# Kernel tuning notes

Hardware: AMD Instinct MI355X
Metric: run time of the kernel (lower is better)

Reference implementation:

```python
import jax, jax.numpy as jnp
import numpy as np

IN_FEATURES = 3
OUT_FEATURES = 256
WEIGHT_SCALE = 1.0
ALPHA = 6.0


def setup_inputs() -> dict:
    key = jax.random.key(0)
    k_x, k_w, k_b, k_mu, k_g = jax.random.split(key, 5)
    B, N = 4, 65536
    # coordinates in [-1, 1], matching mu's init range
    x = jax.random.uniform(k_x, (B, N, IN_FEATURES), jnp.float32, -1.0, 1.0)
    # gamma ~ Gamma(alpha, 1)
    gamma = jax.random.gamma(k_g, ALPHA, (OUT_FEATURES,), jnp.float32)
    # linear weight init (Kaiming-uniform-like) then scaled by weight_scale * sqrt(gamma)
    bound = 1.0 / np.sqrt(IN_FEATURES)
    W = jax.random.uniform(k_w, (OUT_FEATURES, IN_FEATURES), jnp.float32, -bound, bound)
    W = W * (WEIGHT_SCALE * jnp.sqrt(gamma)[:, None])
    # bias ~ U(-pi, pi)
    b = jax.random.uniform(k_b, (OUT_FEATURES,), jnp.float32, -np.pi, np.pi)
    # mu ~ U(-1, 1), stored as (out, in) (the (1,1,out,in) singleton dims are pure broadcast)
    mu = jax.random.uniform(k_mu, (OUT_FEATURES, IN_FEATURES), jnp.float32, -1.0, 1.0)
    return {"x": x, "W": W, "b": b, "mu": mu, "gamma": gamma}


def reference(x, W, b, mu, gamma):
    # linear: (B, N, out)
    lin = jnp.einsum("bnd,od->bno", x, W) + b
    x2 = jnp.sum(x * x, axis=-1, keepdims=True)          # (B, N, 1)
    mu2 = jnp.sum(mu * mu, axis=-1)                       # (out,)
    cross = jnp.einsum("bnd,od->bno", x, mu)             # (B, N, out)
    D = x2 - 2.0 * cross + mu2                            # (B, N, out)
    return jnp.sin(lin) * jnp.exp(-0.5 * D * gamma)
```

## Files before the change

### kernel.cpp

```cpp
#include <hip/hip_runtime.h>


#define OUT_FEATURES 256

__global__ __launch_bounds__(256) void gabor_kernel(
    const float* __restrict__ x,
    const float* __restrict__ W,
    const float* __restrict__ b,
    const float* __restrict__ mu,
    const float* __restrict__ gamma,
    float* __restrict__ out,
    int P)
{
    const int lane        = threadIdx.x & 63;
    const int waveInBlock = threadIdx.x >> 6;
    const int wavesPerBlk = blockDim.x >> 6;
    const int waveId      = blockIdx.x * wavesPerBlk + waveInBlock;
    const int wavesTotal  = gridDim.x * wavesPerBlk;

    const int o = lane << 2;

    float w0[4], w1[4], w2[4], bb[4], m0[4], m1[4], m2[4], mu2s[4], gs[4];
#pragma unroll
    for (int j = 0; j < 4; ++j) {
        const int oj = o + j;
        w0[j] = W[oj * 3 + 0];
        w1[j] = W[oj * 3 + 1];
        w2[j] = W[oj * 3 + 2];
        m0[j] = mu[oj * 3 + 0];
        m1[j] = mu[oj * 3 + 1];
        m2[j] = mu[oj * 3 + 2];
        bb[j] = b[oj];
        gs[j] = -0.5f * gamma[oj];
        mu2s[j] = m0[j] * m0[j] + m1[j] * m1[j] + m2[j] * m2[j];
    }

    for (int p = waveId; p < P; p += wavesTotal) {
        const float x0 = x[p * 3 + 0];
        const float x1 = x[p * 3 + 1];
        const float x2 = x[p * 3 + 2];
        const float xs = x0 * x0 + x1 * x1 + x2 * x2;

        float4 r;
        float* rp = &r.x;
#pragma unroll
        for (int j = 0; j < 4; ++j) {
            const float lin   = fmaf(w0[j], x0, fmaf(w1[j], x1, fmaf(w2[j], x2, bb[j])));
            const float cross = fmaf(m0[j], x0, fmaf(m1[j], x1, m2[j] * x2));
            const float D     = xs - 2.0f * cross + mu2s[j];
            rp[j] = __sinf(lin) * __expf(gs[j] * D);
        }

        *reinterpret_cast<float4*>(out + (size_t)p * OUT_FEATURES + o) = r;
    }
}

extern "C" void kernel_launch(void* const* d_in, const int* in_sizes, int n_in,
                              void* d_out, int out_size, void* d_ws, size_t ws_size,
                              hipStream_t stream) {
    const float* x     = (const float*)d_in[0];
    const float* W     = (const float*)d_in[1];
    const float* b     = (const float*)d_in[2];
    const float* mu    = (const float*)d_in[3];
    const float* gamma = (const float*)d_in[4];
    float* out = (float*)d_out;

    const int P = in_sizes[0] / 3;

    const int blocks = 2048;
    gabor_kernel<<<blocks, 256, 0, stream>>>(x, W, b, mu, gamma, out, P);
}
```

Measured before the change: 283.0 us.

## Use nontemporal output stores, scalar x loads, vector param loads, more blocks

Output stores become nontemporal vector stores so the large write-only result bypasses cache retention. The per-point index is made wave-uniform with readfirstlane so the x loads can become scalar loads. Parameters are now read with 16-byte vector loads. The grid doubles to 4096 blocks and launch bounds request 4 blocks per CU. The kernel is write-bandwidth bound (256 MB of output), so the gain depends mainly on the nontemporal store behaviour.

```diff
diff --git a/kernel.cpp b/kernel.cpp
--- a/kernel.cpp
+++ b/kernel.cpp
@@ -1,9 +1,11 @@
 #include <hip/hip_runtime.h>
 
 
-#define OUT_FEATURES 256
+#define OUT_F 256
 
-__global__ __launch_bounds__(256) void gabor_kernel(
+typedef float v4f __attribute__((ext_vector_type(4)));
+
+__global__ __launch_bounds__(256, 4) void gabor_kernel(
     const float* __restrict__ x,
     const float* __restrict__ W,
     const float* __restrict__ b,
@@ -15,43 +17,49 @@
     const int lane        = threadIdx.x & 63;
     const int waveInBlock = threadIdx.x >> 6;
     const int wavesPerBlk = blockDim.x >> 6;
+    const int wavesTotal  = gridDim.x * wavesPerBlk;
     const int waveId      = blockIdx.x * wavesPerBlk + waveInBlock;
-    const int wavesTotal  = gridDim.x * wavesPerBlk;
 
     const int o = lane << 2;
 
-    float w0[4], w1[4], w2[4], bb[4], m0[4], m1[4], m2[4], mu2s[4], gs[4];
+    float wv[12], mv[12];
+    {
+        const v4f* Wp = (const v4f*)(W + o * 3);
+        const v4f* Mp = (const v4f*)(mu + o * 3);
+#pragma unroll
+        for (int i = 0; i < 3; ++i) {
+            v4f wq = Wp[i], mq = Mp[i];
+#pragma unroll
+            for (int j = 0; j < 4; ++j) { wv[i * 4 + j] = wq[j]; mv[i * 4 + j] = mq[j]; }
+        }
+    }
+    const v4f bq = *(const v4f*)(b + o);
+    const v4f gq = *(const v4f*)(gamma + o);
+
+    float bb[4], gs[4], mu2s[4];
 #pragma unroll
     for (int j = 0; j < 4; ++j) {
-        const int oj = o + j;
-        w0[j] = W[oj * 3 + 0];
-        w1[j] = W[oj * 3 + 1];
-        w2[j] = W[oj * 3 + 2];
-        m0[j] = mu[oj * 3 + 0];
-        m1[j] = mu[oj * 3 + 1];
-        m2[j] = mu[oj * 3 + 2];
-        bb[j] = b[oj];
-        gs[j] = -0.5f * gamma[oj];
-        mu2s[j] = m0[j] * m0[j] + m1[j] * m1[j] + m2[j] * m2[j];
+        bb[j] = bq[j];
+        gs[j] = -0.5f * gq[j];
+        mu2s[j] = mv[j * 3] * mv[j * 3] + mv[j * 3 + 1] * mv[j * 3 + 1] + mv[j * 3 + 2] * mv[j * 3 + 2];
     }
 
     for (int p = waveId; p < P; p += wavesTotal) {
-        const float x0 = x[p * 3 + 0];
-        const float x1 = x[p * 3 + 1];
-        const float x2 = x[p * 3 + 2];
+        const int ps = __builtin_amdgcn_readfirstlane(p);
+        const float x0 = x[ps * 3 + 0];
+        const float x1 = x[ps * 3 + 1];
+        const float x2 = x[ps * 3 + 2];
         const float xs = x0 * x0 + x1 * x1 + x2 * x2;
 
-        float4 r;
-        float* rp = &r.x;
+        v4f r;
 #pragma unroll
         for (int j = 0; j < 4; ++j) {
-            const float lin   = fmaf(w0[j], x0, fmaf(w1[j], x1, fmaf(w2[j], x2, bb[j])));
-            const float cross = fmaf(m0[j], x0, fmaf(m1[j], x1, m2[j] * x2));
+            const float lin   = fmaf(wv[j * 3], x0, fmaf(wv[j * 3 + 1], x1, fmaf(wv[j * 3 + 2], x2, bb[j])));
+            const float cross = fmaf(mv[j * 3], x0, fmaf(mv[j * 3 + 1], x1, mv[j * 3 + 2] * x2));
             const float D     = xs - 2.0f * cross + mu2s[j];
-            rp[j] = __sinf(lin) * __expf(gs[j] * D);
+            r[j] = __sinf(lin) * __expf(gs[j] * D);
         }
-
-        *reinterpret_cast<float4*>(out + (size_t)p * OUT_FEATURES + o) = r;
+        __builtin_nontemporal_store(r, (v4f*)(out + (size_t)p * OUT_F + o));
     }
 }
 
@@ -67,6 +75,5 @@
 
     const int P = in_sizes[0] / 3;
 
-    const int blocks = 2048;
-    gabor_kernel<<<blocks, 256, 0, stream>>>(x, W, b, mu, gamma, out, P);
+    gabor_kernel<<<4096, 256, 0, stream>>>(x, W, b, mu, gamma, out, P);
 }
```

Result: no change. 283.7 us (+0.3%).
